# Kernel tuning notes

Hardware: AMD Instinct MI355X
Metric: run time of the kernel (lower is better)

The kernel has to match this reference:

```python
import jax, jax.numpy as jnp
import numpy as np

D = 128      # flattened state dim (n_dim)
T = 128      # time grid length
N = 32       # quadrature nodes per integral
H = 256      # func MLP hidden
HK = 64      # kernel MLP hidden
ITERS = 3    # IDESolver max_iterations


def setup_inputs() -> dict:
    key = jax.random.key(0)
    ks = jax.random.split(key, 6)
    z0 = jax.random.normal(ks[0], (1, D), jnp.float32)
    t = jnp.linspace(0.0, 1.0, T, dtype=jnp.float32)
    W1 = jax.random.normal(ks[1], (D, H), jnp.float32) / np.float32(np.sqrt(D))
    b1 = jnp.zeros((H,), jnp.float32)
    W2 = jax.random.normal(ks[2], (H, D), jnp.float32) / np.float32(np.sqrt(H))
    b2 = jnp.zeros((D,), jnp.float32)
    Wk1 = jax.random.normal(ks[3], (2, HK), jnp.float32) / np.float32(np.sqrt(2))
    bk1 = jnp.zeros((HK,), jnp.float32)
    # small kernel init keeps the Picard iteration stable
    Wk2 = jax.random.normal(ks[4], (HK, D * D), jnp.float32) * np.float32(0.01 / np.sqrt(HK))
    bk2 = jnp.zeros((D * D,), jnp.float32)
    return dict(z0=z0, t=t, W1=W1, b1=b1, W2=W2, b2=b2,
                Wk1=Wk1, bk1=bk1, Wk2=Wk2, bk2=bk2)


def _spline_coeffs(x, y):
    # natural cubic spline second derivatives M: tridiagonal system, natural BC
    n = x.shape[0]
    h = x[1:] - x[:-1]                       # [T-1]
    A = jnp.zeros((n, n), y.dtype).at[0, 0].set(1.0).at[n - 1, n - 1].set(1.0)
    idx = jnp.arange(1, n - 1)
    A = A.at[idx, idx - 1].set(h[:-1])
    A = A.at[idx, idx].set(2.0 * (h[:-1] + h[1:]))
    A = A.at[idx, idx + 1].set(h[1:])
    slope = (y[1:] - y[:-1]) / h[:, None]
    rhs = jnp.zeros_like(y).at[1:-1].set(6.0 * (slope[1:] - slope[:-1]))
    return jnp.linalg.solve(A, rhs)          # [T, D]


def _spline_eval(x, y, M, q):
    # evaluate spline at flat query points q [Q] -> [Q, D]
    qc = jnp.clip(q, x[0], x[-1])
    i = jnp.clip(jnp.searchsorted(x, qc, side='right') - 1, 0, x.shape[0] - 2)
    h = x[i + 1] - x[i]
    a = (x[i + 1] - qc) / h
    b = (qc - x[i]) / h
    return (a[:, None] * y[i] + b[:, None] * y[i + 1]
            + ((a ** 3 - a)[:, None] * M[i] + (b ** 3 - b)[:, None] * M[i + 1])
            * (h ** 2 / 6.0)[:, None])


def _F(y, W1, b1, W2, b2):
    return jnp.tanh(y @ W1 + b1) @ W2 + b2


def _K(ts, Wk1, bk1, Wk2, bk2):
    # ts [..., 2] -> kernel matrices [..., D, D]
    hden = jnp.tanh(ts @ Wk1 + bk1)
    return (hden @ Wk2 + bk2).reshape(ts.shape[:-1] + (D, D))


def reference(z0, t, W1, b1, W2, b2, Wk1, bk1, Wk2, bk2):
    y0 = z0.reshape(-1)                          # solver state: flattened z0 [D]
    u = jnp.linspace(0.0, 1.0, N, dtype=t.dtype) # unit quad nodes
    wq = jnp.ones((N,), t.dtype).at[0].set(0.5).at[-1].set(0.5)  # trapezoid
    mids = 0.5 * (t[:-1] + t[1:])
    xs = jnp.concatenate([t, mids])              # eval points [P = 2T-1]
    hstep = t[1:] - t[:-1]
    yg = jnp.broadcast_to(y0, (T, D))            # Picard initial guess y^(0)=y0
    for _ in range(ITERS):
        M = _spline_coeffs(t, yg)
        s = xs[:, None] * u[None, :]                              # [P, N], lb=0, ub=x
        ys = _spline_eval(t, yg, M, s.reshape(-1)).reshape(-1, N, D)
        fy = _F(ys, W1, b1, W2, b2)                               # [P, N, D]
        ts = jnp.stack([jnp.broadcast_to(xs[:, None], s.shape), s], -1)
        k = _K(ts, Wk1, bk1, Wk2, bk2)                            # [P, N, D, D]
        integ = jnp.einsum('pnij,pnj->pni', k, fy)
        g = jnp.einsum('pni,n->pi', integ, wq) * (xs / (N - 1))[:, None]  # [P, D]
        g_t, g_m = g[:T], g[T:]
        # Simpson (== RK4 for y-independent RHS) + cumulative integration
        inc = (hstep[:, None] / 6.0) * (g_t[:-1] + 4.0 * g_m + g_t[1:])
        yg = y0[None, :] + jnp.concatenate(
            [jnp.zeros((1, D), yg.dtype), jnp.cumsum(inc, axis=0)])
    return yg[:, None, :]                        # [T, 1, D] like solver.y.unsqueeze(1)
```

## Files before the change

kernel.cpp:

```cpp
#include <hip/hip_runtime.h>
#include <hip/hip_fp16.h>

#define D_  128
#define T_  128
#define P_  255
#define GSZ  32640

#define OFF_YGT   0
#define OFF_COEF  8192
#define OFF_AINV  8704
#define OFF_E     41472
#define OFF_HDW   563712
#define OFF_W1T   828912
#define OFF_W2T   845296
#define OFF_WTT   861680
#define OFF_S     1394160
#define OFF_G2    2459120
#define OFF_CTR   2491760

typedef _Float16 f16;
typedef _Float16 f16x4 __attribute__((ext_vector_type(4)));
typedef float f32x4 __attribute__((ext_vector_type(4)));

__device__ __forceinline__ float tanh_fast(float x) {
  float e = __expf(2.0f * x);
  return 1.0f - 2.0f / (e + 1.0f);
}

__device__ __forceinline__ f16x4 ldfrag(const f16* buf, int row, int kunits,
                                        int kk, int quad) {
  int u = row * kunits + ((kk * 4 + quad) ^ (row & 7));
  return *(const f16x4*)(buf + 4 * u);
}

__global__ __launch_bounds__(256) void k_setup(
    const float* __restrict__ z0, const float* __restrict__ tgrid,
    const float* __restrict__ W1, const float* __restrict__ W2,
    const float* __restrict__ Wk2, const float* __restrict__ bk2,
    __half* __restrict__ ygT, float* __restrict__ coef,
    float* __restrict__ Ainv, __half* __restrict__ W1T,
    __half* __restrict__ W2T, __half* __restrict__ WTC,
    unsigned* __restrict__ ctr) {
  __shared__ __align__(16) unsigned char smem[66560];
  int bid = blockIdx.x, tid = threadIdx.x;
  for (int idx = bid * 256 + tid; idx < 65 * 16384; idx += 256 * 256) {
    int c = idx >> 14, rem = idx & 16383;
    int i = rem >> 7, j = rem & 127;
    float v = (c < 64) ? Wk2[idx] : bk2[rem];
    int kc = c / 5;
    int kr = (c - kc * 5) * 128 + j;
    int kb = kr >> 6, kw = kr & 63;
    WTC[(((kc * 10 + kb) << 7) + i) * 64 + kw] = __float2half(v);
  }
  if (bid == 0) {
    for (int idx = tid; idx < 16384; idx += 256) {
      int grow = idx >> 7, d = idx & 127;
      ygT[d * 128 + grow] = __float2half(z0[d]);
    }
  } else if (bid == 1) {
    for (int idx = tid; idx < 32768; idx += 256) {
      int c = idx >> 7, d = idx & 127;
      W1T[idx] = __float2half(W1[d * 256 + c]);
    }
  } else if (bid == 2) {
    for (int idx = tid; idx < 32768; idx += 256) {
      int j = idx >> 8, c2 = idx & 255;
      W2T[idx] = __float2half(W2[c2 * 128 + j]);
    }
  } else if (bid == 3) {
    if (tid == 0) *ctr = 0u;
  } else if (bid == 255) {
    float* dpL = (float*)smem;
    float* tl  = (float*)(smem + 65024);
    float* cpL = tl + 128;
    float* imL = cpL + 128;
    if (tid < 128) tl[tid] = tgrid[tid];
    __syncthreads();
    if (tid == 0) {
      cpL[0] = 0.0f;
      float cprev = 0.0f;
      for (int i = 1; i <= 126; ++i) {
        float hm = tl[i] - tl[i - 1], hi = tl[i + 1] - tl[i];
        float m = 2.0f * (hm + hi) - hm * cprev;
        float im = 1.0f / m;
        imL[i] = im;
        cprev = hi * im;
        cpL[i] = cprev;
      }
    }
    if (tid < 127) coef[256 + tid] = 1.0f / (tl[tid + 1] - tl[tid]);
    __syncthreads();
    if (tid < 128) {
      int d = tid;
      float dprev = (d == 0) ? 1.0f : 0.0f;
      dpL[d] = dprev;
      for (int i = 1; i <= 126; ++i) {
        float rhs = (i == d) ? 1.0f : 0.0f;
        float hm = tl[i] - tl[i - 1];
        dprev = (rhs - hm * dprev) * imL[i];
        dpL[i * 128 + d] = dprev;
      }
      float x = (d == 127) ? 1.0f : 0.0f;
      Ainv[127 * 128 + d] = x;
      for (int i = 126; i >= 0; --i) {
        x = dpL[i * 128 + d] - cpL[i] * x;
        Ainv[i * 128 + d] = x;
      }
    }
  }
}

__global__ __launch_bounds__(512) void k_fused(
    __half* __restrict__ E, __half* __restrict__ HDW,
    const __half* __restrict__ ygT,
    const __half* __restrict__ W1T, const __half* __restrict__ W2T,
    const float* __restrict__ b1, const float* __restrict__ b2,
    __half* __restrict__ Sq, float* __restrict__ g,
    const float* __restrict__ tgrid, const float* __restrict__ Wk1,
    const float* __restrict__ bk1, const float* __restrict__ coef,
    const float* __restrict__ Ainv, int it) {
  __shared__ __align__(16) unsigned char smem[65536];
  __shared__ float tl[128], ihL[128];
  __shared__ float sn[32], an[32], bn[32], cA[32], cB[32];
  __shared__ int idn[32];
  f16* RW = (f16*)smem;
  f16* RA = (f16*)(smem + 32768);
  f16* RB = (f16*)(smem + 40960);
  f16* RC = (f16*)(smem + 49152);
  int p = blockIdx.x, tid = threadIdx.x;
  int wv = tid >> 6, l = tid & 63, quad = l >> 4, r = l & 15;

  if (tid < 128) g[p * 128 + tid] = 0.0f;
  if (p == 0) {
    for (int z = tid; z < 8320; z += 512) {
      int kcS = z / 640, kr = z - kcS * 640;
      Sq[kcS * 163840 + 255 * 640 + kr] = __float2half(0.0f);
    }
  }

  if (it == 0) {
    if (tid < 128) tl[tid] = tgrid[tid];
    if (tid < 127) ihL[tid] = coef[256 + tid];
    __syncthreads();
    float xp = (p < T_) ? tl[p] : 0.5f * (tl[p - T_] + tl[p - T_ + 1]);
    if (tid < 32) {
      int n = tid;
      float u = (float)n * (1.0f / 31.0f);
      float q = xp * u;
      float qc = fminf(fmaxf(q, tl[0]), tl[127]);
      int i = (int)floorf(qc * 127.0f);
      i = max(0, min(126, i));
      while (i > 0 && qc < tl[i]) --i;
      while (i < 126 && qc >= tl[i + 1]) ++i;
      float h = tl[i + 1] - tl[i];
      float aa = (tl[i + 1] - qc) / h, bb = (qc - tl[i]) / h;
      sn[n] = q; idn[n] = i; an[n] = aa; bn[n] = bb;
      float h26 = h * h * (1.0f / 6.0f);
      cA[n] = (aa * aa * aa - aa) * h26;
      cB[n] = (bb * bb * bb - bb) * h26;
    }
    __syncthreads();
    #pragma unroll
    for (int pass = 0; pass < 8; ++pass) {
      int n = pass * 4 + (tid >> 7);
      int b = tid & 127;
      int i = idn[n];
      float Gi = 0.0f, Gi1 = 0.0f;
      if (b >= 2) {
        float w = 6.0f * ihL[b - 1];
        Gi  += Ainv[i * 128 + b - 1] * w;
        Gi1 += Ainv[(i + 1) * 128 + b - 1] * w;
      }
      if (b >= 1 && b <= 126) {
        float w = -6.0f * (ihL[b - 1] + ihL[b]);
        Gi  += Ainv[i * 128 + b] * w;
        Gi1 += Ainv[(i + 1) * 128 + b] * w;
      }
      if (b <= 125) {
        float w = 6.0f * ihL[b];
        Gi  += Ainv[i * 128 + b + 1] * w;
        Gi1 += Ainv[(i + 1) * 128 + b + 1] * w;
      }
      float v = cA[n] * Gi + cB[n] * Gi1;
      if (b == i) v += an[n];
      if (b == i + 1) v += bn[n];
      E[(p * 32 + n) * 128 + b] = __float2half(v);
    }
    #pragma unroll
    for (int k = 0; k < 5; ++k) {
      int idx = k * 512 + tid;
      if (idx < 2080) {
        int c = idx >> 5, n = idx & 31;
        float wq = (n == 0 || n == 31) ? 0.5f : 1.0f;
        float v = (c < 64)
            ? wq * tanh_fast(fmaf(xp, Wk1[c], fmaf(sn[n], Wk1[64 + c], bk1[c])))
            : wq;
        HDW[p * 2080 + idx] = __float2half(v);
      }
    }
    __syncthreads();
  }

  uint2 pf[8];
  uint2 pfh[2];
  {
    const uint2* s1 = (const uint2*)W1T;
    #pragma unroll
    for (int k = 0; k < 8; ++k) pf[k] = s1[k * 512 + tid];
  }
  {
    const uint2* src = (const uint2*)ygT;
    uint2* dst = (uint2*)RW;
    #pragma unroll
    for (int k = 0; k < 8; ++k) {
      int idx = k * 512 + tid;
      int row = idx >> 5, k4 = idx & 31;
      dst[row * 32 + (k4 ^ (row & 7))] = src[idx];
    }
    const uint2* se = (const uint2*)(E + p * 4096);
    uint2* da = (uint2*)RA;
    #pragma unroll
    for (int k = 0; k < 2; ++k) {
      int idx = k * 512 + tid;
      int row = idx >> 5, k4 = idx & 31;
      da[row * 32 + (k4 ^ (row & 7))] = se[idx];
    }
  }
  __syncthreads();
  for (int tt = wv; tt < 16; tt += 8) {
    int mt = tt >> 3, nt = tt & 7;
    f32x4 acc = {0.f, 0.f, 0.f, 0.f};
    #pragma unroll
    for (int kk = 0; kk < 8; ++kk) {
      f16x4 av = ldfrag(RA, mt * 16 + r, 32, kk, quad);
      f16x4 bv = ldfrag(RW, nt * 16 + r, 32, kk, quad);
      acc = __builtin_amdgcn_mfma_f32_16x16x16f16(av, bv, acc, 0, 0, 0);
    }
    int col = nt * 16 + r;
    #pragma unroll
    for (int i = 0; i < 4; ++i) {
      int row = mt * 16 + quad * 4 + i;
      RB[row * 128 + (col ^ ((row & 7) << 2))] = (f16)acc[i];
    }
  }
  __syncthreads();
  {
    uint2* dst = (uint2*)RW;
    #pragma unroll
    for (int k = 0; k < 8; ++k) {
      int idx = k * 512 + tid;
      int row = idx >> 5, k4 = idx & 31;
      dst[row * 32 + (k4 ^ (row & 7))] = pf[k];
    }
    const uint2* s1 = (const uint2*)(W1T + 16384);
    #pragma unroll
    for (int k = 0; k < 8; ++k) pf[k] = s1[k * 512 + tid];
  }
  __syncthreads();
  for (int tt = wv; tt < 16; tt += 8) {
    int mt = tt >> 3, nt = tt & 7;
    f32x4 acc = {0.f, 0.f, 0.f, 0.f};
    #pragma unroll
    for (int kk = 0; kk < 8; ++kk) {
      f16x4 av = ldfrag(RB, mt * 16 + r, 32, kk, quad);
      f16x4 bv = ldfrag(RW, nt * 16 + r, 32, kk, quad);
      acc = __builtin_amdgcn_mfma_f32_16x16x16f16(av, bv, acc, 0, 0, 0);
    }
    int colg = nt * 16 + r;
    float bias = b1[colg];
    #pragma unroll
    for (int i = 0; i < 4; ++i) {
      int row = mt * 16 + quad * 4 + i;
      RC[row * 256 + (colg ^ ((row & 7) << 2))] = (f16)tanh_fast(acc[i] + bias);
    }
  }
  __syncthreads();
  {
    uint2* dst = (uint2*)RW;
    #pragma unroll
    for (int k = 0; k < 8; ++k) {
      int idx = k * 512 + tid;
      int row = idx >> 5, k4 = idx & 31;
      dst[row * 32 + (k4 ^ (row & 7))] = pf[k];
    }
    const uint2* sh_ = (const uint2*)(HDW + p * 2080);
    #pragma unroll
    for (int k = 0; k < 2; ++k) {
      int idx = k * 512 + tid;
      if (idx < 640) pfh[k] = (idx < 520) ? sh_[idx] : make_uint2(0u, 0u);
    }
    const uint2* s2 = (const uint2*)W2T;
    #pragma unroll
    for (int k = 0; k < 8; ++k) pf[k] = s2[k * 512 + tid];
  }
  __syncthreads();
  for (int tt = wv; tt < 16; tt += 8) {
    int mt = tt >> 3, nt = tt & 7;
    f32x4 acc = {0.f, 0.f, 0.f, 0.f};
    #pragma unroll
    for (int kk = 0; kk < 8; ++kk) {
      f16x4 av = ldfrag(RB, mt * 16 + r, 32, kk, quad);
      f16x4 bv = ldfrag(RW, nt * 16 + r, 32, kk, quad);
      acc = __builtin_amdgcn_mfma_f32_16x16x16f16(av, bv, acc, 0, 0, 0);
    }
    int colg = 128 + nt * 16 + r;
    float bias = b1[colg];
    #pragma unroll
    for (int i = 0; i < 4; ++i) {
      int row = mt * 16 + quad * 4 + i;
      RC[row * 256 + (colg ^ ((row & 7) << 2))] = (f16)tanh_fast(acc[i] + bias);
    }
  }
  __syncthreads();
  {
    uint2* db = (uint2*)RB;
    #pragma unroll
    for (int k = 0; k < 2; ++k) {
      int idx = k * 512 + tid;
      if (idx < 640) {
        int row = idx >> 3, k4 = idx & 7;
        db[row * 8 + (k4 ^ (row & 7))] = pfh[k];
      }
    }
    uint2* dst = (uint2*)RW;
    #pragma unroll
    for (int k = 0; k < 8; ++k) {
      int idx = k * 512 + tid;
      int row = idx >> 6, k4 = idx & 63;
      dst[row * 64 + (k4 ^ (row & 7))] = pf[k];
    }
    const uint2* s2 = (const uint2*)(W2T + 16384);
    #pragma unroll
    for (int k = 0; k < 8; ++k) pf[k] = s2[k * 512 + tid];
  }
  __syncthreads();
  for (int tt = wv; tt < 8; tt += 8) {
    int mt = tt >> 2, nt = tt & 3;
    f32x4 acc = {0.f, 0.f, 0.f, 0.f};
    #pragma unroll
    for (int kk = 0; kk < 16; ++kk) {
      f16x4 av = ldfrag(RC, mt * 16 + r, 64, kk, quad);
      f16x4 bv = ldfrag(RW, nt * 16 + r, 64, kk, quad);
      acc = __builtin_amdgcn_mfma_f32_16x16x16f16(av, bv, acc, 0, 0, 0);
    }
    int jg = nt * 16 + r;
    float bias = b2[jg];
    #pragma unroll
    for (int i = 0; i < 4; ++i) {
      int n = mt * 16 + quad * 4 + i;
      RA[jg * 32 + (n ^ ((jg & 7) << 2))] = (f16)(acc[i] + bias);
    }
  }
  __syncthreads();
  {
    uint2* dst = (uint2*)RW;
    #pragma unroll
    for (int k = 0; k < 8; ++k) {
      int idx = k * 512 + tid;
      int row = idx >> 6, k4 = idx & 63;
      dst[row * 64 + (k4 ^ (row & 7))] = pf[k];
    }
  }
  __syncthreads();
  for (int tt = wv; tt < 8; tt += 8) {
    int mt = tt >> 2, nt = tt & 3;
    f32x4 acc = {0.f, 0.f, 0.f, 0.f};
    #pragma unroll
    for (int kk = 0; kk < 16; ++kk) {
      f16x4 av = ldfrag(RC, mt * 16 + r, 64, kk, quad);
      f16x4 bv = ldfrag(RW, nt * 16 + r, 64, kk, quad);
      acc = __builtin_amdgcn_mfma_f32_16x16x16f16(av, bv, acc, 0, 0, 0);
    }
    int jg = 64 + nt * 16 + r;
    float bias = b2[jg];
    #pragma unroll
    for (int i = 0; i < 4; ++i) {
      int n = mt * 16 + quad * 4 + i;
      RA[jg * 32 + (n ^ ((jg & 7) << 2))] = (f16)(acc[i] + bias);
    }
  }
  __syncthreads();
  for (int tt = wv; tt < 40; tt += 8) {
    int mt = tt >> 3, nt = tt & 7;
    f32x4 acc = {0.f, 0.f, 0.f, 0.f};
    #pragma unroll
    for (int kk = 0; kk < 2; ++kk) {
      f16x4 av = ldfrag(RB, mt * 16 + r, 8, kk, quad);
      f16x4 bv = ldfrag(RA, nt * 16 + r, 8, kk, quad);
      acc = __builtin_amdgcn_mfma_f32_16x16x16f16(av, bv, acc, 0, 0, 0);
    }
    #pragma unroll
    for (int i = 0; i < 4; ++i) {
      int c = mt * 16 + quad * 4 + i;
      if (c < 65) {
        int col = nt * 16 + r;
        int kcS = c / 5;
        int kr = (c - kcS * 5) * 128 + col;
        Sq[kcS * 163840 + p * 640 + kr] = __float2half(acc[i]);
      }
    }
  }
}

__global__ __launch_bounds__(256) void k_gemmM(
    const __half* __restrict__ Sq, const __half* __restrict__ WTC,
    float* __restrict__ g, const float* __restrict__ t,
    const float* __restrict__ z0, __half* __restrict__ ygT,
    float* __restrict__ out, unsigned* __restrict__ ctr, int wout) {
  __shared__ __align__(16) unsigned char smem[65280];
  __shared__ unsigned lastFlag;
  uint2* Asw  = (uint2*)smem;
  uint2* Bsw0 = (uint2*)(smem + 20480);
  uint2* Bsw1 = (uint2*)(smem + 36864);
  int mt = blockIdx.x;
  int kc = blockIdx.y;
  int tid = threadIdx.x;
  int wv = tid >> 6, l = tid & 63, quad = l >> 4, r = l & 15;
  int p0 = mt * 16;
  int rowT = tid >> 4, u4lo = tid & 15;
  {
    const uint2* srcA = (const uint2*)(Sq + kc * 163840 + (p0 + rowT) * 640) + u4lo;
    #pragma unroll
    for (int pass = 0; pass < 10; ++pass) {
      int u4 = pass * 16 + u4lo;
      Asw[rowT * 160 + (u4 ^ (rowT & 7))] = srcA[pass * 16];
    }
  }
  const uint2* bbase = (const uint2*)WTC + kc * 10 * 2048;
  #pragma unroll
  for (int pass = 0; pass < 8; ++pass) {
    int idx = pass * 256 + tid;
    int row = idx >> 4, u4 = idx & 15;
    Bsw0[row * 16 + (u4 ^ (row & 7))] = bbase[idx];
  }
  __syncthreads();
  f32x4 acc0 = {0.f, 0.f, 0.f, 0.f}, acc1 = {0.f, 0.f, 0.f, 0.f};
  int n0 = wv * 32;
  const f16* Af = (const f16*)Asw;
  for (int kb = 0; kb < 10; ++kb) {
    const f16* Bf = (const f16*)((kb & 1) ? Bsw1 : Bsw0);
    uint2* nxtB = (kb & 1) ? Bsw0 : Bsw1;
    uint2 pf[8];
    if (kb < 9) {
      const uint2* srcN = bbase + (kb + 1) * 2048;
      #pragma unroll
      for (int pass = 0; pass < 8; ++pass) pf[pass] = srcN[pass * 256 + tid];
    }
    #pragma unroll
    for (int kk = 0; kk < 4; ++kk) {
      int kg4 = kb * 16 + kk * 4 + quad;
      f16x4 av = *(const f16x4*)(Af + 4 * (r * 160 + (kg4 ^ (r & 7))));
      int nr0 = n0 + r, nr1 = n0 + 16 + r;
      f16x4 b0 = *(const f16x4*)(Bf + 4 * (nr0 * 16 + ((kk * 4 + quad) ^ (nr0 & 7))));
      f16x4 b1 = *(const f16x4*)(Bf + 4 * (nr1 * 16 + ((kk * 4 + quad) ^ (nr1 & 7))));
      acc0 = __builtin_amdgcn_mfma_f32_16x16x16f16(av, b0, acc0, 0, 0, 0);
      acc1 = __builtin_amdgcn_mfma_f32_16x16x16f16(av, b1, acc1, 0, 0, 0);
    }
    if (kb < 9) {
      #pragma unroll
      for (int pass = 0; pass < 8; ++pass) {
        int idx = pass * 256 + tid;
        int row = idx >> 4, u4 = idx & 15;
        nxtB[row * 16 + (u4 ^ (row & 7))] = pf[pass];
      }
    }
    __syncthreads();
  }
  #pragma unroll
  for (int i = 0; i < 4; ++i) {
    int p = p0 + quad * 4 + i;
    if (p < 255) {
      atomicAdd(&g[p * 128 + n0 + r], acc0[i]);
      atomicAdd(&g[p * 128 + n0 + 16 + r], acc1[i]);
    }
  }
  __threadfence();
  if (tid == 0) {
    unsigned old = atomicAdd(ctr, 1u);
    lastFlag = (old == 207u) ? 1u : 0u;
    if (lastFlag) *ctr = 0u;
  }
  __syncthreads();
  if (!lastFlag) return;
  __threadfence();
  float* incL = (float*)smem;
  for (int idx = tid; idx < 127 * 128; idx += 256) {
    int k = idx >> 7, d = idx & 127;
    float tk = t[k], tk1 = t[k + 1];
    float h = tk1 - tk;
    float sct  = tk * (1.0f / 31.0f);
    float scm  = 0.5f * (tk + tk1) * (1.0f / 31.0f);
    float sct1 = tk1 * (1.0f / 31.0f);
    incL[idx] = h * (1.0f / 6.0f) *
        (g[k * 128 + d] * sct + 4.0f * g[(T_ + k) * 128 + d] * scm +
         g[(k + 1) * 128 + d] * sct1);
  }
  __syncthreads();
  if (tid < 128) {
    int d = tid;
    float acc = z0[d];
    ygT[d * 128] = __float2half(acc);
    if (wout) out[d] = acc;
    #pragma unroll 4
    for (int k = 0; k < 127; ++k) {
      acc += incL[k * 128 + d];
      ygT[d * 128 + k + 1] = __float2half(acc);
      if (wout) out[(k + 1) * 128 + d] = acc;
    }
  }
}

extern "C" void kernel_launch(void* const* d_in, const int* in_sizes, int n_in,
                              void* d_out, int out_size, void* d_ws, size_t ws_size,
                              hipStream_t stream) {
  const float* z0  = (const float*)d_in[0];
  const float* t   = (const float*)d_in[1];
  const float* W1  = (const float*)d_in[2];
  const float* b1  = (const float*)d_in[3];
  const float* W2  = (const float*)d_in[4];
  const float* b2  = (const float*)d_in[5];
  const float* Wk1 = (const float*)d_in[6];
  const float* bk1 = (const float*)d_in[7];
  const float* Wk2 = (const float*)d_in[8];
  const float* bk2 = (const float*)d_in[9];
  float* out = (float*)d_out;
  float* ws  = (float*)d_ws;

  __half*   ygT  = (__half*)(ws + OFF_YGT);
  float*    coef = ws + OFF_COEF;
  float*    Ainv = ws + OFF_AINV;
  __half*   E    = (__half*)(ws + OFF_E);
  __half*   HDW  = (__half*)(ws + OFF_HDW);
  __half*   W1T  = (__half*)(ws + OFF_W1T);
  __half*   W2T  = (__half*)(ws + OFF_W2T);
  __half*   WTC  = (__half*)(ws + OFF_WTT);
  __half*   Sq   = (__half*)(ws + OFF_S);
  float*    g    = ws + OFF_G2;
  unsigned* ctr  = (unsigned*)(ws + OFF_CTR);

  k_setup<<<dim3(256), dim3(256), 0, stream>>>(z0, t, W1, W2, Wk2, bk2,
                                               ygT, coef, Ainv, W1T, W2T, WTC,
                                               ctr);
  for (int it = 0; it < 3; ++it) {
    k_fused<<<dim3(255), dim3(512), 0, stream>>>(E, HDW, ygT, W1T, W2T,
                                                 b1, b2, Sq, g, t, Wk1, bk1,
                                                 coef, Ainv, it);
    k_gemmM<<<dim3(16, 13), dim3(256), 0, stream>>>(Sq, WTC, g, t, z0, ygT, out,
                                                    ctr, (it == 2) ? 1 : 0);
  }
}
```

Baseline: 180.1 us.

## Pre-swizzle MFMA operands in global memory and load fragments directly

Stores ygT, W1, W2 and E in global memory already arranged in MFMA fragment order, so each lane can read its f16x4 operand straight from global or L2. This removes the LDS staging round trips and most of the __syncthreads barriers in k_fused, and the GEMM stages are merged into single loops over wider tile ranges. LDS use per block drops from 64KB to 32KB, which may allow more blocks per CU. In exchange, weight fragments are re-read from L2 by every block with less latency hiding, and the ygF writes in the scan loop become scattered.

```diff
diff --git a/kernel.cpp b/kernel.cpp
--- a/kernel.cpp
+++ b/kernel.cpp
@@ -6,13 +6,13 @@
 #define P_  255
 #define GSZ  32640
 
-#define OFF_YGT   0
+#define OFF_YGF   0
 #define OFF_COEF  8192
 #define OFF_AINV  8704
 #define OFF_E     41472
 #define OFF_HDW   563712
-#define OFF_W1T   828912
-#define OFF_W2T   845296
+#define OFF_W1F   828912
+#define OFF_W2F   845296
 #define OFF_WTT   861680
 #define OFF_S     1394160
 #define OFF_G2    2459120
@@ -37,9 +37,9 @@
     const float* __restrict__ z0, const float* __restrict__ tgrid,
     const float* __restrict__ W1, const float* __restrict__ W2,
     const float* __restrict__ Wk2, const float* __restrict__ bk2,
-    __half* __restrict__ ygT, float* __restrict__ coef,
-    float* __restrict__ Ainv, __half* __restrict__ W1T,
-    __half* __restrict__ W2T, __half* __restrict__ WTC,
+    __half* __restrict__ ygF, float* __restrict__ coef,
+    float* __restrict__ Ainv, __half* __restrict__ W1F,
+    __half* __restrict__ W2F, __half* __restrict__ WTC,
     unsigned* __restrict__ ctr) {
   __shared__ __align__(16) unsigned char smem[66560];
   int bid = blockIdx.x, tid = threadIdx.x;
@@ -54,18 +54,23 @@
   }
   if (bid == 0) {
     for (int idx = tid; idx < 16384; idx += 256) {
-      int grow = idx >> 7, d = idx & 127;
-      ygT[d * 128 + grow] = __float2half(z0[d]);
+      int l2 = (idx >> 2) & 63, blk = idx >> 8;
+      int nt = blk >> 3, rr = l2 & 15;
+      ygF[idx] = __float2half(z0[nt * 16 + rr]);
     }
   } else if (bid == 1) {
     for (int idx = tid; idx < 32768; idx += 256) {
-      int c = idx >> 7, d = idx & 127;
-      W1T[idx] = __float2half(W1[d * 256 + c]);
+      int j = idx & 3, l2 = (idx >> 2) & 63, blk = idx >> 8;
+      int nt = blk >> 3, kk = blk & 7, rr = l2 & 15, qd = l2 >> 4;
+      int c = nt * 16 + rr, d = kk * 16 + qd * 4 + j;
+      W1F[idx] = __float2half(W1[d * 256 + c]);
     }
   } else if (bid == 2) {
     for (int idx = tid; idx < 32768; idx += 256) {
-      int j = idx >> 8, c2 = idx & 255;
-      W2T[idx] = __float2half(W2[c2 * 128 + j]);
+      int j = idx & 3, l2 = (idx >> 2) & 63, blk = idx >> 8;
+      int nt = blk >> 4, kk = blk & 15, rr = l2 & 15, qd = l2 >> 4;
+      int jcol = nt * 16 + rr, c = kk * 16 + qd * 4 + j;
+      W2F[idx] = __float2half(W2[c * 128 + jcol]);
     }
   } else if (bid == 3) {
     if (tid == 0) *ctr = 0u;
@@ -111,22 +116,21 @@
 }
 
 __global__ __launch_bounds__(512) void k_fused(
-    __half* __restrict__ E, __half* __restrict__ HDW,
-    const __half* __restrict__ ygT,
-    const __half* __restrict__ W1T, const __half* __restrict__ W2T,
+    __half* __restrict__ EF, __half* __restrict__ HDW,
+    const __half* __restrict__ ygF,
+    const __half* __restrict__ W1F, const __half* __restrict__ W2F,
     const float* __restrict__ b1, const float* __restrict__ b2,
     __half* __restrict__ Sq, float* __restrict__ g,
     const float* __restrict__ tgrid, const float* __restrict__ Wk1,
     const float* __restrict__ bk1, const float* __restrict__ coef,
     const float* __restrict__ Ainv, int it) {
-  __shared__ __align__(16) unsigned char smem[65536];
+  __shared__ __align__(16) unsigned char smem[32768];
   __shared__ float tl[128], ihL[128];
   __shared__ float sn[32], an[32], bn[32], cA[32], cB[32];
   __shared__ int idn[32];
-  f16* RW = (f16*)smem;
-  f16* RA = (f16*)(smem + 32768);
-  f16* RB = (f16*)(smem + 40960);
-  f16* RC = (f16*)(smem + 49152);
+  f16* RA = (f16*)smem;
+  f16* RB = (f16*)(smem + 8192);
+  f16* RC = (f16*)(smem + 16384);
   int p = blockIdx.x, tid = threadIdx.x;
   int wv = tid >> 6, l = tid & 63, quad = l >> 4, r = l & 15;
 
@@ -184,7 +188,10 @@
       float v = cA[n] * Gi + cB[n] * Gi1;
       if (b == i) v += an[n];
       if (b == i + 1) v += bn[n];
-      E[(p * 32 + n) * 128 + b] = __float2half(v);
+      int mtE = n >> 4, rrE = n & 15;
+      int kkE = b >> 4, qdE = (b >> 2) & 3, jE = b & 3;
+      EF[p * 4096 + ((((mtE * 8 + kkE) * 64 + qdE * 16 + rrE)) << 2) + jE] =
+          __float2half(v);
     }
     #pragma unroll
     for (int k = 0; k < 5; ++k) {
@@ -201,39 +208,23 @@
     __syncthreads();
   }
 
-  uint2 pf[8];
   uint2 pfh[2];
   {
-    const uint2* s1 = (const uint2*)W1T;
-    #pragma unroll
-    for (int k = 0; k < 8; ++k) pf[k] = s1[k * 512 + tid];
-  }
-  {
-    const uint2* src = (const uint2*)ygT;
-    uint2* dst = (uint2*)RW;
-    #pragma unroll
-    for (int k = 0; k < 8; ++k) {
-      int idx = k * 512 + tid;
-      int row = idx >> 5, k4 = idx & 31;
-      dst[row * 32 + (k4 ^ (row & 7))] = src[idx];
-    }
-    const uint2* se = (const uint2*)(E + p * 4096);
-    uint2* da = (uint2*)RA;
+    const uint2* sh_ = (const uint2*)(HDW + p * 2080);
     #pragma unroll
     for (int k = 0; k < 2; ++k) {
       int idx = k * 512 + tid;
-      int row = idx >> 5, k4 = idx & 31;
-      da[row * 32 + (k4 ^ (row & 7))] = se[idx];
-    }
-  }
-  __syncthreads();
+      if (idx < 640) pfh[k] = (idx < 520) ? sh_[idx] : make_uint2(0u, 0u);
+    }
+  }
+  const f16* efp = (const f16*)EF + p * 4096;
   for (int tt = wv; tt < 16; tt += 8) {
     int mt = tt >> 3, nt = tt & 7;
     f32x4 acc = {0.f, 0.f, 0.f, 0.f};
     #pragma unroll
     for (int kk = 0; kk < 8; ++kk) {
-      f16x4 av = ldfrag(RA, mt * 16 + r, 32, kk, quad);
-      f16x4 bv = ldfrag(RW, nt * 16 + r, 32, kk, quad);
+      f16x4 av = *(const f16x4*)(efp + (((mt * 8 + kk) * 64 + l) << 2));
+      f16x4 bv = *(const f16x4*)((const f16*)ygF + (((nt * 8 + kk) * 64 + l) << 2));
       acc = __builtin_amdgcn_mfma_f32_16x16x16f16(av, bv, acc, 0, 0, 0);
     }
     int col = nt * 16 + r;
@@ -244,66 +235,16 @@
     }
   }
   __syncthreads();
-  {
-    uint2* dst = (uint2*)RW;
-    #pragma unroll
-    for (int k = 0; k < 8; ++k) {
-      int idx = k * 512 + tid;
-      int row = idx >> 5, k4 = idx & 31;
-      dst[row * 32 + (k4 ^ (row & 7))] = pf[k];
-    }
-    const uint2* s1 = (const uint2*)(W1T + 16384);
-    #pragma unroll
-    for (int k = 0; k < 8; ++k) pf[k] = s1[k * 512 + tid];
-  }
-  __syncthreads();
-  for (int tt = wv; tt < 16; tt += 8) {
-    int mt = tt >> 3, nt = tt & 7;
+  for (int tt = wv; tt < 32; tt += 8) {
+    int mt = tt >> 4, nt = tt & 15;
     f32x4 acc = {0.f, 0.f, 0.f, 0.f};
     #pragma unroll
     for (int kk = 0; kk < 8; ++kk) {
       f16x4 av = ldfrag(RB, mt * 16 + r, 32, kk, quad);
-      f16x4 bv = ldfrag(RW, nt * 16 + r, 32, kk, quad);
+      f16x4 bv = *(const f16x4*)((const f16*)W1F + (((nt * 8 + kk) * 64 + l) << 2));
       acc = __builtin_amdgcn_mfma_f32_16x16x16f16(av, bv, acc, 0, 0, 0);
     }
     int colg = nt * 16 + r;
-    float bias = b1[colg];
-    #pragma unroll
-    for (int i = 0; i < 4; ++i) {
-      int row = mt * 16 + quad * 4 + i;
-      RC[row * 256 + (colg ^ ((row & 7) << 2))] = (f16)tanh_fast(acc[i] + bias);
-    }
-  }
-  __syncthreads();
-  {
-    uint2* dst = (uint2*)RW;
-    #pragma unroll
-    for (int k = 0; k < 8; ++k) {
-      int idx = k * 512 + tid;
-      int row = idx >> 5, k4 = idx & 31;
-      dst[row * 32 + (k4 ^ (row & 7))] = pf[k];
-    }
-    const uint2* sh_ = (const uint2*)(HDW + p * 2080);
-    #pragma unroll
-    for (int k = 0; k < 2; ++k) {
-      int idx = k * 512 + tid;
-      if (idx < 640) pfh[k] = (idx < 520) ? sh_[idx] : make_uint2(0u, 0u);
-    }
-    const uint2* s2 = (const uint2*)W2T;
-    #pragma unroll
-    for (int k = 0; k < 8; ++k) pf[k] = s2[k * 512 + tid];
-  }
-  __syncthreads();
-  for (int tt = wv; tt < 16; tt += 8) {
-    int mt = tt >> 3, nt = tt & 7;
-    f32x4 acc = {0.f, 0.f, 0.f, 0.f};
-    #pragma unroll
-    for (int kk = 0; kk < 8; ++kk) {
-      f16x4 av = ldfrag(RB, mt * 16 + r, 32, kk, quad);
-      f16x4 bv = ldfrag(RW, nt * 16 + r, 32, kk, quad);
-      acc = __builtin_amdgcn_mfma_f32_16x16x16f16(av, bv, acc, 0, 0, 0);
-    }
-    int colg = 128 + nt * 16 + r;
     float bias = b1[colg];
     #pragma unroll
     for (int i = 0; i < 4; ++i) {
@@ -322,56 +263,17 @@
         db[row * 8 + (k4 ^ (row & 7))] = pfh[k];
       }
     }
-    uint2* dst = (uint2*)RW;
-    #pragma unroll
-    for (int k = 0; k < 8; ++k) {
-      int idx = k * 512 + tid;
-      int row = idx >> 6, k4 = idx & 63;
-      dst[row * 64 + (k4 ^ (row & 7))] = pf[k];
-    }
-    const uint2* s2 = (const uint2*)(W2T + 16384);
-    #pragma unroll
-    for (int k = 0; k < 8; ++k) pf[k] = s2[k * 512 + tid];
-  }
-  __syncthreads();
-  for (int tt = wv; tt < 8; tt += 8) {
-    int mt = tt >> 2, nt = tt & 3;
+  }
+  for (int tt = wv; tt < 16; tt += 8) {
+    int mt = tt >> 3, nt = tt & 7;
     f32x4 acc = {0.f, 0.f, 0.f, 0.f};
     #pragma unroll
     for (int kk = 0; kk < 16; ++kk) {
       f16x4 av = ldfrag(RC, mt * 16 + r, 64, kk, quad);
-      f16x4 bv = ldfrag(RW, nt * 16 + r, 64, kk, quad);
+      f16x4 bv = *(const f16x4*)((const f16*)W2F + (((nt * 16 + kk) * 64 + l) << 2));
       acc = __builtin_amdgcn_mfma_f32_16x16x16f16(av, bv, acc, 0, 0, 0);
     }
     int jg = nt * 16 + r;
-    float bias = b2[jg];
-    #pragma unroll
-    for (int i = 0; i < 4; ++i) {
-      int n = mt * 16 + quad * 4 + i;
-      RA[jg * 32 + (n ^ ((jg & 7) << 2))] = (f16)(acc[i] + bias);
-    }
-  }
-  __syncthreads();
-  {
-    uint2* dst = (uint2*)RW;
-    #pragma unroll
-    for (int k = 0; k < 8; ++k) {
-      int idx = k * 512 + tid;
-      int row = idx >> 6, k4 = idx & 63;
-      dst[row * 64 + (k4 ^ (row & 7))] = pf[k];
-    }
-  }
-  __syncthreads();
-  for (int tt = wv; tt < 8; tt += 8) {
-    int mt = tt >> 2, nt = tt & 3;
-    f32x4 acc = {0.f, 0.f, 0.f, 0.f};
-    #pragma unroll
-    for (int kk = 0; kk < 16; ++kk) {
-      f16x4 av = ldfrag(RC, mt * 16 + r, 64, kk, quad);
-      f16x4 bv = ldfrag(RW, nt * 16 + r, 64, kk, quad);
-      acc = __builtin_amdgcn_mfma_f32_16x16x16f16(av, bv, acc, 0, 0, 0);
-    }
-    int jg = 64 + nt * 16 + r;
     float bias = b2[jg];
     #pragma unroll
     for (int i = 0; i < 4; ++i) {
@@ -405,7 +307,7 @@
 __global__ __launch_bounds__(256) void k_gemmM(
     const __half* __restrict__ Sq, const __half* __restrict__ WTC,
     float* __restrict__ g, const float* __restrict__ t,
-    const float* __restrict__ z0, __half* __restrict__ ygT,
+    const float* __restrict__ z0, __half* __restrict__ ygF,
     float* __restrict__ out, unsigned* __restrict__ ctr, int wout) {
   __shared__ __align__(16) unsigned char smem[65280];
   __shared__ unsigned lastFlag;
@@ -497,15 +399,18 @@
   }
   __syncthreads();
   if (tid < 128) {
-    int d = tid;
+    int d = tid, ntF = d >> 4, rrF = d & 15;
     float acc = z0[d];
-    ygT[d * 128] = __float2half(acc);
+    ygF[((ntF * 8) * 64 + rrF) << 2] = __float2half(acc);
     if (wout) out[d] = acc;
     #pragma unroll 4
     for (int k = 0; k < 127; ++k) {
       acc += incL[k * 128 + d];
-      ygT[d * 128 + k + 1] = __float2half(acc);
-      if (wout) out[(k + 1) * 128 + d] = acc;
+      int kp = k + 1;
+      int kkF = kp >> 4, qdF = (kp >> 2) & 3, jF = kp & 3;
+      ygF[((((ntF * 8 + kkF) * 64 + qdF * 16 + rrF)) << 2) + jF] =
+          __float2half(acc);
+      if (wout) out[kp * 128 + d] = acc;
     }
   }
 }
@@ -526,26 +431,26 @@
   float* out = (float*)d_out;
   float* ws  = (float*)d_ws;
 
-  __half*   ygT  = (__half*)(ws + OFF_YGT);
+  __half*   ygF  = (__half*)(ws + OFF_YGF);
   float*    coef = ws + OFF_COEF;
   float*    Ainv = ws + OFF_AINV;
-  __half*   E    = (__half*)(ws + OFF_E);
+  __half*   EF   = (__half*)(ws + OFF_E);
   __half*   HDW  = (__half*)(ws + OFF_HDW);
-  __half*   W1T  = (__half*)(ws + OFF_W1T);
-  __half*   W2T  = (__half*)(ws + OFF_W2T);
+  __half*   W1F  = (__half*)(ws + OFF_W1F);
+  __half*   W2F  = (__half*)(ws + OFF_W2F);
   __half*   WTC  = (__half*)(ws + OFF_WTT);
   __half*   Sq   = (__half*)(ws + OFF_S);
   float*    g    = ws + OFF_G2;
   unsigned* ctr  = (unsigned*)(ws + OFF_CTR);
 
   k_setup<<<dim3(256), dim3(256), 0, stream>>>(z0, t, W1, W2, Wk2, bk2,
-                                               ygT, coef, Ainv, W1T, W2T, WTC,
+                                               ygF, coef, Ainv, W1F, W2F, WTC,
                                                ctr);
   for (int it = 0; it < 3; ++it) {
-    k_fused<<<dim3(255), dim3(512), 0, stream>>>(E, HDW, ygT, W1T, W2T,
+    k_fused<<<dim3(255), dim3(512), 0, stream>>>(EF, HDW, ygF, W1F, W2F,
                                                  b1, b2, Sq, g, t, Wk1, bk1,
                                                  coef, Ainv, it);
-    k_gemmM<<<dim3(16, 13), dim3(256), 0, stream>>>(Sq, WTC, g, t, z0, ygT, out,
+    k_gemmM<<<dim3(16, 13), dim3(256), 0, stream>>>(Sq, WTC, g, t, z0, ygF, out,
                                                     ctr, (it == 2) ? 1 : 0);
   }
 }
```

After: 167.4 us (median of 2 runs). -7.1%, faster.
